# Kernel optimization log

Hardware: AMD Instinct MI355X
Metric: run time of the kernel (lower is better)

## Reference

```python
import jax, jax.numpy as jnp
import numpy as np

N_CONCEPTS = 32
KMEANS_ITERS = 10   # fixed Lloyd iterations (stand-in for fit-to-convergence)
CC_ITERS = 20       # label-propagation + pointer-jumping iterations (>= ~2*log2(N))


def setup_inputs() -> dict:
    key = jax.random.key(0)
    k1, k2, k3, k4 = jax.random.split(key, 4)
    B, N, F = 16, 512, 256
    x = jax.random.normal(k1, (B, N, F), dtype=jnp.float32)
    # sparse symmetric 0/1 adjacency, no self loops, avg degree ~20
    u = jax.random.uniform(k2, (B, N, N))
    a = (u < 0.02).astype(jnp.float32)
    adj = jnp.clip(a + jnp.swapaxes(a, 1, 2), 0.0, 1.0)
    adj = adj * (1.0 - jnp.eye(N, dtype=jnp.float32))
    mask = jnp.ones((B, N), dtype=bool)
    s = 1.0 / np.sqrt(F)
    W1 = jax.random.normal(k3, (F, F), jnp.float32) * s
    b1 = jnp.zeros((F,), jnp.float32)
    W2 = jax.random.normal(k4, (F, F), jnp.float32) * s
    b2 = jnp.zeros((F,), jnp.float32)
    return {"x": x, "adj": adj, "mask": mask, "W1": W1, "b1": b1, "W2": W2, "b2": b2}


def _gcn(x, adj, mask, W, b):
    # DenseGCNConv: D^-1/2 (A+I) D^-1/2 (X W) + b, masked
    N = x.shape[1]
    h = x @ W
    a = adj + jnp.eye(N, dtype=adj.dtype)
    d = jnp.clip(a.sum(-1), 1.0, None) ** -0.5
    a = d[:, :, None] * a * d[:, None, :]
    out = jnp.einsum('bij,bjf->bif', a, h) + b
    return jnp.where(mask[:, :, None], out, 0.0)


def _kmeans_fit_predict(pts, k):
    # Lloyd iterations, euclidean; deterministic init = first k points
    cent = pts[:k]
    p2 = (pts * pts).sum(-1)
    for _ in range(KMEANS_ITERS):
        d2 = p2[:, None] - 2.0 * pts @ cent.T + (cent * cent).sum(-1)[None]
        assign = jnp.argmin(d2, -1)
        sums = jax.ops.segment_sum(pts, assign, num_segments=k)
        cnt = jax.ops.segment_sum(jnp.ones_like(p2), assign, num_segments=k)
        cent = jnp.where(cnt[:, None] > 0, sums / jnp.maximum(cnt, 1.0)[:, None], cent)
    d2 = p2[:, None] - 2.0 * pts @ cent.T + (cent * cent).sum(-1)[None]
    return jnp.argmin(d2, -1)


def _components(adj_same, mask):
    # connected components of same-concept subgraph; returns 1-based cluster ids (0 = masked)
    B, N, _ = adj_same.shape
    idx = jnp.arange(N)
    labels = jnp.broadcast_to(idx[None, :], (B, N))
    A = adj_same > 0

    def step(lab, _):
        nb = jnp.where(A, lab[:, None, :], N)        # [B,N,N] neighbor labels
        lab = jnp.minimum(lab, nb.min(-1))           # hook to min neighbor
        lab = jnp.take_along_axis(lab, lab, axis=1)  # pointer jump
        lab = jnp.take_along_axis(lab, lab, axis=1)
        return lab, None

    labels, _ = jax.lax.scan(step, labels, None, length=CC_ITERS)
    is_root = mask & (labels == idx[None, :])
    ids = jnp.cumsum(is_root.astype(jnp.int32), axis=1)   # consecutive ids, 1-based at roots
    assign = jnp.take_along_axis(ids, labels, axis=1)
    return jnp.where(mask, assign, 0)


def _forward(x, adj, mask, W1, b1, W2, b2):
    B, N, F = x.shape
    h = jax.nn.relu(_gcn(x, adj, mask, W1, b1))
    h = jax.nn.relu(_gcn(h, adj, mask, W2, b2))
    # mask is all-true -> x[mask] is a flat reshape
    pts = jax.lax.stop_gradient(h.reshape(B * N, F))
    concepts = _kmeans_fit_predict(pts, N_CONCEPTS).reshape(B, N)
    adj_same = jnp.where(concepts[:, :, None] == concepts[:, None, :], adj, 0.0)
    assignments = _components(adj_same, mask)           # [B,N] in {0..N}
    seg_sum = jax.vmap(lambda v, s: jax.ops.segment_sum(v, s, num_segments=N + 1))
    x_new = seg_sum(h, assignments)[:, 1:, :]           # drop reserved cluster 0
    seg_max = jax.vmap(lambda v, s: jax.ops.segment_max(v, s, num_segments=N + 1))
    adj_r = jnp.maximum(seg_max(adj, assignments), 0.0)[:, 1:, :]                      # pool rows
    adj_new = jnp.maximum(seg_max(jnp.swapaxes(adj_r, 1, 2), assignments), 0.0)[:, 1:, :]
    adj_new = jnp.swapaxes(adj_new, 1, 2)                                              # pool cols
    num_clusters = assignments.max(-1)
    mask_new = jnp.arange(N)[None, :] < num_clusters[:, None]
    return x_new, adj_new, concepts, h, mask_new


def reference(x, adj, mask, W1, b1, W2, b2):
    return _forward(x, adj, mask, W1, b1, W2, b2)
```

## Files before the change

### kernel.cpp

```cpp
#include <hip/hip_runtime.h>
#include <cstdint>
#include <cstddef>

#define BB 16
#define NN 512
#define FF 256
#define NC 32
#define KITERS 10
#define CCITERS 20
#define MAXD 96
#define FMAXD 64

typedef __attribute__((ext_vector_type(4))) double double4_t;

__global__ __launch_bounds__(64) void build_adjbits(const float* __restrict__ adj,
                                                    unsigned long long* __restrict__ adjbits,
                                                    double* __restrict__ dinv,
                                                    unsigned short* __restrict__ nbr,
                                                    int* __restrict__ degv) {
  int i = blockIdx.x, b = blockIdx.y, lane = threadIdx.x;
  const float* row = adj + ((size_t)(b * NN + i)) * NN;
  unsigned long long lmask = (1ULL << lane) - 1ULL;
  int base = 0;
#pragma unroll
  for (int q = 0; q < 8; ++q) {
    bool pred = (row[q * 64 + lane] != 0.0f);
    unsigned long long m = __ballot(pred ? 1 : 0);
    if (lane == 0) adjbits[((size_t)(b * NN + i)) * 8 + q] = m;
    if (pred) {
      int pos = base + __popcll(m & lmask);
      if (pos < MAXD) nbr[((size_t)(b * NN + i)) * MAXD + pos] = (unsigned short)(q * 64 + lane);
    }
    base += __popcll(m);
  }
  if (lane == 0) {
    degv[b * NN + i] = base;
    double tot = (double)base + 1.0;
    dinv[b * NN + i] = 1.0 / sqrt(tot);
  }
}

__global__ __launch_bounds__(256) void gemm_scale(const float* __restrict__ X,
                                                  const float* __restrict__ W,
                                                  const double* __restrict__ dinv,
                                                  float* __restrict__ Y) {
  __shared__ float As[16][68];
  __shared__ float Bs[16][64];
  int bm = blockIdx.x, bn = blockIdx.y, b = blockIdx.z;
  int tid = threadIdx.x;
  int tx = tid & 15, ty = tid >> 4;
  const float* Xb = X + (size_t)b * NN * FF;
  float* Yb = Y + (size_t)b * NN * FF;
  double acc[4][4] = {};
  for (int kt = 0; kt < FF; kt += 16) {
    {
      int m = tid >> 2, kq = (tid & 3) * 4;
      const float4 v = *(const float4*)&Xb[(size_t)(bm * 64 + m) * FF + kt + kq];
      As[kq + 0][m] = v.x; As[kq + 1][m] = v.y; As[kq + 2][m] = v.z; As[kq + 3][m] = v.w;
    }
    {
      int k = tid >> 4, n4 = (tid & 15) * 4;
      *(float4*)&Bs[k][n4] = *(const float4*)&W[(size_t)(kt + k) * FF + bn * 64 + n4];
    }
    __syncthreads();
#pragma unroll
    for (int k = 0; k < 16; ++k) {
      float4 a = *(const float4*)&As[k][ty * 4];
      float4 bv = *(const float4*)&Bs[k][tx * 4];
      double ax = a.x, ay = a.y, az = a.z, aw = a.w;
      double bx = bv.x, by = bv.y, bz = bv.z, bw = bv.w;
      acc[0][0] += ax * bx; acc[0][1] += ax * by; acc[0][2] += ax * bz; acc[0][3] += ax * bw;
      acc[1][0] += ay * bx; acc[1][1] += ay * by; acc[1][2] += ay * bz; acc[1][3] += ay * bw;
      acc[2][0] += az * bx; acc[2][1] += az * by; acc[2][2] += az * bz; acc[2][3] += az * bw;
      acc[3][0] += aw * bx; acc[3][1] += aw * by; acc[3][2] += aw * bz; acc[3][3] += aw * bw;
    }
    __syncthreads();
  }
#pragma unroll
  for (int i = 0; i < 4; ++i) {
    int row = bm * 64 + ty * 4 + i;
    double di = dinv[b * NN + row];
    float4 v;
    v.x = (float)(di * acc[i][0]); v.y = (float)(di * acc[i][1]);
    v.z = (float)(di * acc[i][2]); v.w = (float)(di * acc[i][3]);
    *(float4*)&Yb[(size_t)row * FF + bn * 64 + tx * 4] = v;
  }
}

__global__ __launch_bounds__(256) void spmv_relu(const float* __restrict__ Y,
                                                 const unsigned short* __restrict__ nbr,
                                                 const int* __restrict__ degv,
                                                 const unsigned long long* __restrict__ adjbits,
                                                 const double* __restrict__ dinv,
                                                 const float* __restrict__ bias,
                                                 float* __restrict__ H) {
  int i = blockIdx.x, b = blockIdx.y, f = threadIdx.x;
  int row = b * NN + i;
  const float* Yb = Y + (size_t)b * NN * FF;
  double z = (double)Yb[(size_t)i * FF + f];
  int deg = degv[row];
  if (deg <= MAXD) {
    const unsigned short* lst = nbr + (size_t)row * MAXD;
    int n = 0;
    for (; n + 4 <= deg; n += 4) {
      int j0 = lst[n], j1 = lst[n + 1], j2 = lst[n + 2], j3 = lst[n + 3];
      float v0 = Yb[(size_t)j0 * FF + f];
      float v1 = Yb[(size_t)j1 * FF + f];
      float v2 = Yb[(size_t)j2 * FF + f];
      float v3 = Yb[(size_t)j3 * FF + f];
      z += (double)v0; z += (double)v1; z += (double)v2; z += (double)v3;
    }
    for (; n < deg; ++n) z += (double)Yb[(size_t)lst[n] * FF + f];
  } else {
    const unsigned long long* brow = adjbits + (size_t)row * 8;
    for (int q = 0; q < 8; ++q) {
      unsigned long long bits = brow[q];
      while (bits) {
        int j = (q << 6) + __builtin_ctzll(bits);
        bits &= bits - 1;
        z += (double)Yb[(size_t)j * FF + f];
      }
    }
  }
  double h = dinv[row] * z + (double)bias[f];
  H[((size_t)row) * FF + f] = (h > 0.0) ? (float)h : 0.0f;
}

__global__ __launch_bounds__(256) void p2cent_kernel(const float* __restrict__ pts,
                                                     double* __restrict__ p2,
                                                     double* __restrict__ cent,
                                                     double* __restrict__ c2) {
  __shared__ double red[256];
  int p = blockIdx.x, t = threadIdx.x;
  double v = (double)pts[(size_t)p * FF + t];
  if (p < NC) cent[p * FF + t] = v;
  red[t] = v * v;
  __syncthreads();
  for (int s = 128; s; s >>= 1) { if (t < s) red[t] += red[t + s]; __syncthreads(); }
  if (t == 0) {
    p2[p] = red[0];
    if (p < NC) c2[p] = red[0];
  }
}

__global__ __launch_bounds__(256) void kmeans_assign(const float* __restrict__ pts,
                                                     const double* __restrict__ cent,
                                                     const double* __restrict__ c2,
                                                     const double* __restrict__ p2,
                                                     int* __restrict__ assignI,
                                                     double* __restrict__ part,
                                                     int* __restrict__ cntp,
                                                     float* __restrict__ conceptsF) {
  __shared__ float ps[32][260];
  __shared__ double csT[256][35];
  __shared__ double d2s[32][33];
  __shared__ double want[3];
  __shared__ double probe_raw[2][2];
  __shared__ int as[32];
  __shared__ int hyp;
  int g = blockIdx.x, tid = threadIdx.x;

  for (int r = 0; r < 32; ++r) ps[r][tid] = pts[(size_t)(g * 32 + r) * FF + tid];
  for (int rep = 0; rep < 32; ++rep) csT[tid][rep] = cent[rep * FF + tid];
  __syncthreads();

  int lane = tid & 63, w = tid >> 6;
  int prow = (w >> 1) * 16, ccol = (w & 1) * 16;
  int r16 = lane & 15, kg = lane >> 4;
  double4_t acc = {0.0, 0.0, 0.0, 0.0};
  for (int kt = 0; kt < FF; kt += 4) {
    double a = (double)ps[prow + r16][kt + kg];
    double bv = csT[kt + kg][ccol + r16];
    acc = __builtin_amdgcn_mfma_f64_16x16x4f64(a, bv, acc, 0, 0, 0);
  }
  if (tid < 2) { probe_raw[tid][0] = acc[0]; probe_raw[tid][1] = acc[1]; }
  __syncthreads();

  if (tid < 192) {
    int pw = tid >> 6;
    int pr = (pw == 2) ? 1 : 0;
    int pc = (pw == 1) ? 1 : 0;
    double partial = 0.0;
#pragma unroll
    for (int kk = 0; kk < 4; ++kk)
      partial += (double)ps[pr][lane * 4 + kk] * csT[lane * 4 + kk][pc];
    for (int off = 32; off; off >>= 1) partial += __shfl_xor(partial, off, 64);
    if (lane == 0) want[pw] = partial;
  }
  __syncthreads();
  if (tid == 0) {
    double w00 = want[0], w01 = want[1], w10 = want[2];
    double m00 = probe_raw[0][0], mA = probe_raw[1][0], mB = probe_raw[0][1];
    auto near = [](double a, double b) { return fabs(a - b) <= 1e-9 * (1.0 + fabs(b)); };
    bool ok00 = near(m00, w00);
    bool h1 = ok00 && near(mA, w01) && near(mB, w10);
    bool h2 = ok00 && near(mB, w01) && near(mA, w10);
    hyp = h1 ? 0 : (h2 ? 1 : 2);
  }
  __syncthreads();
  int hh = hyp;
  if (hh == 0) {
#pragma unroll
    for (int ii = 0; ii < 4; ++ii) {
      int row = prow + kg * 4 + ii, col = ccol + r16;
      d2s[row][col] = (p2[g * 32 + row] - 2.0 * acc[ii]) + c2[col];
    }
  } else if (hh == 1) {
#pragma unroll
    for (int ii = 0; ii < 4; ++ii) {
      int row = prow + r16, col = ccol + kg * 4 + ii;
      d2s[row][col] = (p2[g * 32 + row] - 2.0 * acc[ii]) + c2[col];
    }
  }
  __syncthreads();
  if (hh == 2) {
    int p0 = tid >> 4, c0 = tid & 15;
    double a00 = 0., a01 = 0., a10 = 0., a11 = 0.;
    for (int k = 0; k < FF; ++k) {
      double pa = (double)ps[p0][k], pb = (double)ps[p0 + 16][k];
      double ca = csT[k][c0], cb = csT[k][c0 + 16];
      a00 += pa * ca; a01 += pa * cb; a10 += pb * ca; a11 += pb * cb;
    }
    double pp0 = p2[g * 32 + p0], pp1 = p2[g * 32 + p0 + 16];
    double cc0 = c2[c0], cc1 = c2[c0 + 16];
    d2s[p0][c0]           = (pp0 - 2.0 * a00) + cc0;
    d2s[p0][c0 + 16]      = (pp0 - 2.0 * a01) + cc1;
    d2s[p0 + 16][c0]      = (pp1 - 2.0 * a10) + cc0;
    d2s[p0 + 16][c0 + 16] = (pp1 - 2.0 * a11) + cc1;
  }
  __syncthreads();

  if (tid < 32) {
    double m = d2s[tid][0];
    int idx = 0;
    for (int c = 1; c < 32; ++c) {
      double v = d2s[tid][c];
      if (v < m) { m = v; idx = c; }
    }
    as[tid] = idx;
    assignI[g * 32 + tid] = idx;
    if (conceptsF) conceptsF[g * 32 + tid] = (float)idx;
  }
  double* accm = &csT[0][0];
  for (int r = 0; r < 32; ++r) accm[r * 258 + tid] = 0.0;
  __syncthreads();
  for (int r = 0; r < 32; ++r) { int s = as[r]; accm[s * 258 + tid] += (double)ps[r][tid]; }
  for (int r = 0; r < 32; ++r) part[((size_t)r * 256 + g) * FF + tid] = accm[r * 258 + tid];
  if (tid < 32) {
    int c = 0;
    for (int r = 0; r < 32; ++r) c += (as[r] == tid) ? 1 : 0;
    cntp[tid * 256 + g] = c;
  }
}

__global__ __launch_bounds__(256) void kmeans_update(const double* __restrict__ part,
                                                     const int* __restrict__ cntp,
                                                     double* __restrict__ cent,
                                                     double* __restrict__ c2) {
  __shared__ double red[256];
  int k = blockIdx.x, f = threadIdx.x;
  double s0 = 0., s1 = 0., s2 = 0., s3 = 0.;
  for (int g = 0; g < 256; g += 4) {
    s0 += part[((size_t)k * 256 + g + 0) * FF + f];
    s1 += part[((size_t)k * 256 + g + 1) * FF + f];
    s2 += part[((size_t)k * 256 + g + 2) * FF + f];
    s3 += part[((size_t)k * 256 + g + 3) * FF + f];
  }
  double acc = (s0 + s1) + (s2 + s3);
  int cnt = 0;
  for (int g = 0; g < 256; ++g) cnt += cntp[k * 256 + g];
  double v = (cnt > 0) ? (acc / (double)cnt) : cent[k * FF + f];
  cent[k * FF + f] = v;
  red[f] = v * v;
  __syncthreads();
  for (int s = 128; s; s >>= 1) { if (f < s) red[f] += red[f + s]; __syncthreads(); }
  if (f == 0) c2[k] = red[0];
}

__global__ __launch_bounds__(64) void build_bits(const unsigned long long* __restrict__ adjbits,
                                                 const int* __restrict__ concepts,
                                                 unsigned short* __restrict__ flistT,
                                                 int* __restrict__ fdegv) {
  int i = blockIdx.x, b = blockIdx.y, lane = threadIdx.x;
  int ci = concepts[b * NN + i];
  unsigned long long lmask = (1ULL << lane) - 1ULL;
  int base = 0;
#pragma unroll
  for (int q = 0; q < 8; ++q) {
    unsigned long long wbits = adjbits[((size_t)(b * NN + i)) * 8 + q];
    bool pred = ((wbits >> lane) & 1ULL) && (concepts[b * NN + q * 64 + lane] == ci);
    unsigned long long m = __ballot(pred ? 1 : 0);
    if (pred) {
      int pos = base + __popcll(m & lmask);
      if (pos < FMAXD) flistT[((size_t)b * FMAXD + pos) * NN + i] = (unsigned short)(q * 64 + lane);
    }
    base += __popcll(m);
  }
  if (lane == 0) fdegv[b * NN + i] = base;
}

__global__ __launch_bounds__(512) void components_kernel(const unsigned short* __restrict__ flistT,
                                                         const int* __restrict__ fdegv,
                                                         int* __restrict__ comp,
                                                         float* __restrict__ maskF) {
  __shared__ unsigned short LT[FMAXD][512];
  __shared__ int lab[512];
  __shared__ int ids[512];
  int b = blockIdx.x, t = threadIdx.x;
  for (int n = 0; n < FMAXD; ++n) LT[n][t] = flistT[((size_t)b * FMAXD + n) * NN + t];
  int fd = fdegv[b * NN + t];
  if (fd > FMAXD) fd = FMAXD;
  lab[t] = t;
  __syncthreads();
  for (int it = 0; it < CCITERS; ++it) {
    int old = lab[t];
    int m = old;
    for (int n = 0; n < fd; ++n) m = min(m, lab[LT[n][t]]);
    __syncthreads();
    lab[t] = m;
    __syncthreads();
    int a = lab[m];
    __syncthreads();
    lab[t] = a;
    __syncthreads();
    int a2 = lab[a];
    __syncthreads();
    lab[t] = a2;
    int changed = (a2 != old) ? 1 : 0;
    if (__syncthreads_or(changed) == 0) break;
  }
  if (t == 0) {
    int run = 0;
    for (int i = 0; i < 512; ++i) { run += (lab[i] == i) ? 1 : 0; ids[i] = run; }
  }
  __syncthreads();
  comp[b * NN + t] = ids[lab[t]];
  maskF[b * NN + t] = (t < ids[511]) ? 1.0f : 0.0f;
}

__global__ __launch_bounds__(256) void xnew_kernel(const float* __restrict__ H,
                                                   const int* __restrict__ comp,
                                                   float* __restrict__ xnew) {
  int i = blockIdx.x, b = blockIdx.y, f = threadIdx.x;
  int s = comp[b * NN + i] - 1;
  atomicAdd(&xnew[((size_t)(b * NN + s)) * FF + f], H[((size_t)(b * NN + i)) * FF + f]);
}

__global__ __launch_bounds__(64) void adjnew_kernel(const unsigned long long* __restrict__ adjbits,
                                                    const int* __restrict__ comp,
                                                    float* __restrict__ out) {
  int b = blockIdx.y, lane = threadIdx.x;
  int i = blockIdx.x * 8 + (lane >> 3);
  int q = lane & 7;
  unsigned long long bits = adjbits[((size_t)(b * NN + i)) * 8 + q];
  if (!bits) return;
  int si = comp[b * NN + i] - 1;
  float* ob = out + (size_t)b * NN * NN;
  while (bits) {
    int j = (q << 6) + __builtin_ctzll(bits);
    bits &= bits - 1;
    int sj = comp[b * NN + j] - 1;
    ob[(size_t)si * NN + sj] = 1.0f;
  }
}

extern "C" void kernel_launch(void* const* d_in, const int* in_sizes, int n_in,
                              void* d_out, int out_size, void* d_ws, size_t ws_size,
                              hipStream_t stream) {
  (void)in_sizes; (void)n_in; (void)out_size; (void)ws_size;
  const float* x   = (const float*)d_in[0];
  const float* adj = (const float*)d_in[1];
  const float* W1 = (const float*)d_in[3];
  const float* b1 = (const float*)d_in[4];
  const float* W2 = (const float*)d_in[5];
  const float* b2 = (const float*)d_in[6];

  float* out = (float*)d_out;
  float* xnew      = out;
  float* adjnew    = out + 2097152;
  float* conceptsF = out + 6291456;
  float* hout      = out + 6299648;
  float* maskF     = out + 8396800;

  char* ws = (char*)d_ws;
  double* dinv = (double*)(ws + 0);
  float*  y    = (float*)(ws + 65536);
  float*  h1   = (float*)(ws + 8454144);
  double* cent = (double*)(ws + 16842752);
  double* c2   = (double*)(ws + 16908288);
  double* p2   = (double*)(ws + 16908544);
  unsigned long long* adjbits = (unsigned long long*)(ws + 16974080);
  int* assignI = (int*)(ws + 17498368);
  int* cntp    = (int*)(ws + 17531136);
  int* comp    = (int*)(ws + 17563904);
  int* degv    = assignI;
  double* part = (double*)adjnew;
  unsigned short* nbr = (unsigned short*)xnew;
  unsigned short* flistT = (unsigned short*)h1;
  int* fdegv = (int*)(ws + 8454144 + 2097152);

  build_adjbits<<<dim3(NN, BB), 64, 0, stream>>>(adj, adjbits, dinv, nbr, degv);

  gemm_scale<<<dim3(8, 4, BB), 256, 0, stream>>>(x, W1, dinv, y);
  spmv_relu<<<dim3(NN, BB), 256, 0, stream>>>(y, nbr, degv, adjbits, dinv, b1, h1);
  gemm_scale<<<dim3(8, 4, BB), 256, 0, stream>>>(h1, W2, dinv, y);
  spmv_relu<<<dim3(NN, BB), 256, 0, stream>>>(y, nbr, degv, adjbits, dinv, b2, hout);

  hipMemsetAsync(xnew, 0, (size_t)2097152 * sizeof(float), stream);

  const float* pts = hout;
  p2cent_kernel<<<BB * NN, 256, 0, stream>>>(pts, p2, cent, c2);
  for (int it = 0; it < KITERS; ++it) {
    kmeans_assign<<<256, 256, 0, stream>>>(pts, cent, c2, p2, assignI, part, cntp, nullptr);
    kmeans_update<<<NC, 256, 0, stream>>>(part, cntp, cent, c2);
  }
  kmeans_assign<<<256, 256, 0, stream>>>(pts, cent, c2, p2, assignI, part, cntp, conceptsF);

  hipMemsetAsync(adjnew, 0, (size_t)4194304 * sizeof(float), stream);

  build_bits<<<dim3(NN, BB), 64, 0, stream>>>(adjbits, assignI, flistT, fdegv);
  components_kernel<<<BB, 512, 0, stream>>>(flistT, fdegv, comp, maskF);

  xnew_kernel<<<dim3(NN, BB), 256, 0, stream>>>(hout, comp, xnew);
  adjnew_kernel<<<dim3(64, BB), 64, 0, stream>>>(adjbits, comp, adjnew);
}
```

Before: 695.4 us.

## Split k-means centroid update across feature chunks and compute centroid norms in assign

```diff
diff --git a/kernel.cpp b/kernel.cpp
--- a/kernel.cpp
+++ b/kernel.cpp
@@ -128,8 +128,7 @@
 
 __global__ __launch_bounds__(256) void p2cent_kernel(const float* __restrict__ pts,
                                                      double* __restrict__ p2,
-                                                     double* __restrict__ cent,
-                                                     double* __restrict__ c2) {
+                                                     double* __restrict__ cent) {
   __shared__ double red[256];
   int p = blockIdx.x, t = threadIdx.x;
   double v = (double)pts[(size_t)p * FF + t];
@@ -137,15 +136,11 @@
   red[t] = v * v;
   __syncthreads();
   for (int s = 128; s; s >>= 1) { if (t < s) red[t] += red[t + s]; __syncthreads(); }
-  if (t == 0) {
-    p2[p] = red[0];
-    if (p < NC) c2[p] = red[0];
-  }
+  if (t == 0) p2[p] = red[0];
 }
 
 __global__ __launch_bounds__(256) void kmeans_assign(const float* __restrict__ pts,
                                                      const double* __restrict__ cent,
-                                                     const double* __restrict__ c2,
                                                      const double* __restrict__ p2,
                                                      int* __restrict__ assignI,
                                                      double* __restrict__ part,
@@ -154,6 +149,7 @@
   __shared__ float ps[32][260];
   __shared__ double csT[256][35];
   __shared__ double d2s[32][33];
+  __shared__ double c2s[32];
   __shared__ double want[3];
   __shared__ double probe_raw[2][2];
   __shared__ int as[32];
@@ -163,6 +159,12 @@
   for (int r = 0; r < 32; ++r) ps[r][tid] = pts[(size_t)(g * 32 + r) * FF + tid];
   for (int rep = 0; rep < 32; ++rep) csT[tid][rep] = cent[rep * FF + tid];
   __syncthreads();
+
+  if (tid < 32) {
+    double s = 0.;
+    for (int k = 0; k < FF; ++k) { double cv = csT[k][tid]; s += cv * cv; }
+    c2s[tid] = s;
+  }
 
   int lane = tid & 63, w = tid >> 6;
   int prow = (w >> 1) * 16, ccol = (w & 1) * 16;
@@ -203,13 +205,13 @@
 #pragma unroll
     for (int ii = 0; ii < 4; ++ii) {
       int row = prow + kg * 4 + ii, col = ccol + r16;
-      d2s[row][col] = (p2[g * 32 + row] - 2.0 * acc[ii]) + c2[col];
+      d2s[row][col] = (p2[g * 32 + row] - 2.0 * acc[ii]) + c2s[col];
     }
   } else if (hh == 1) {
 #pragma unroll
     for (int ii = 0; ii < 4; ++ii) {
       int row = prow + r16, col = ccol + kg * 4 + ii;
-      d2s[row][col] = (p2[g * 32 + row] - 2.0 * acc[ii]) + c2[col];
+      d2s[row][col] = (p2[g * 32 + row] - 2.0 * acc[ii]) + c2s[col];
     }
   }
   __syncthreads();
@@ -222,7 +224,7 @@
       a00 += pa * ca; a01 += pa * cb; a10 += pb * ca; a11 += pb * cb;
     }
     double pp0 = p2[g * 32 + p0], pp1 = p2[g * 32 + p0 + 16];
-    double cc0 = c2[c0], cc1 = c2[c0 + 16];
+    double cc0 = c2s[c0], cc1 = c2s[c0 + 16];
     d2s[p0][c0]           = (pp0 - 2.0 * a00) + cc0;
     d2s[p0][c0 + 16]      = (pp0 - 2.0 * a01) + cc1;
     d2s[p0 + 16][c0]      = (pp1 - 2.0 * a10) + cc0;
@@ -255,26 +257,29 @@
 
 __global__ __launch_bounds__(256) void kmeans_update(const double* __restrict__ part,
                                                      const int* __restrict__ cntp,
-                                                     double* __restrict__ cent,
-                                                     double* __restrict__ c2) {
-  __shared__ double red[256];
-  int k = blockIdx.x, f = threadIdx.x;
-  double s0 = 0., s1 = 0., s2 = 0., s3 = 0.;
-  for (int g = 0; g < 256; g += 4) {
-    s0 += part[((size_t)k * 256 + g + 0) * FF + f];
-    s1 += part[((size_t)k * 256 + g + 1) * FF + f];
-    s2 += part[((size_t)k * 256 + g + 2) * FF + f];
-    s3 += part[((size_t)k * 256 + g + 3) * FF + f];
-  }
-  double acc = (s0 + s1) + (s2 + s3);
-  int cnt = 0;
-  for (int g = 0; g < 256; ++g) cnt += cntp[k * 256 + g];
-  double v = (cnt > 0) ? (acc / (double)cnt) : cent[k * FF + f];
-  cent[k * FF + f] = v;
-  red[f] = v * v;
-  __syncthreads();
-  for (int s = 128; s; s >>= 1) { if (f < s) red[f] += red[f + s]; __syncthreads(); }
-  if (f == 0) c2[k] = red[0];
+                                                     double* __restrict__ cent) {
+  __shared__ double red[8][33];
+  __shared__ int cred[256];
+  int k = blockIdx.x, fc = blockIdx.y;
+  int tid = threadIdx.x;
+  int fl = tid & 31, gl = tid >> 5;
+  int f = fc * 32 + fl;
+  double s = 0.;
+  for (int gg = 0; gg < 32; ++gg) {
+    int g = gl + gg * 8;
+    s += part[((size_t)k * 256 + g) * FF + f];
+  }
+  red[gl][fl] = s;
+  cred[tid] = cntp[k * 256 + tid];
+  __syncthreads();
+  for (int q = 128; q; q >>= 1) { if (tid < q) cred[tid] += cred[tid + q]; __syncthreads(); }
+  if (gl == 0) {
+    double acc = 0.;
+    for (int q = 0; q < 8; ++q) acc += red[q][fl];
+    int cnt = cred[0];
+    double v = (cnt > 0) ? (acc / (double)cnt) : cent[k * FF + f];
+    cent[k * FF + f] = v;
+  }
 }
 
 __global__ __launch_bounds__(64) void build_bits(const unsigned long long* __restrict__ adjbits,
@@ -387,7 +392,6 @@
   float*  y    = (float*)(ws + 65536);
   float*  h1   = (float*)(ws + 8454144);
   double* cent = (double*)(ws + 16842752);
-  double* c2   = (double*)(ws + 16908288);
   double* p2   = (double*)(ws + 16908544);
   unsigned long long* adjbits = (unsigned long long*)(ws + 16974080);
   int* assignI = (int*)(ws + 17498368);
@@ -409,12 +413,12 @@
   hipMemsetAsync(xnew, 0, (size_t)2097152 * sizeof(float), stream);
 
   const float* pts = hout;
-  p2cent_kernel<<<BB * NN, 256, 0, stream>>>(pts, p2, cent, c2);
+  p2cent_kernel<<<BB * NN, 256, 0, stream>>>(pts, p2, cent);
   for (int it = 0; it < KITERS; ++it) {
-    kmeans_assign<<<256, 256, 0, stream>>>(pts, cent, c2, p2, assignI, part, cntp, nullptr);
-    kmeans_update<<<NC, 256, 0, stream>>>(part, cntp, cent, c2);
-  }
-  kmeans_assign<<<256, 256, 0, stream>>>(pts, cent, c2, p2, assignI, part, cntp, conceptsF);
+    kmeans_assign<<<256, 256, 0, stream>>>(pts, cent, p2, assignI, part, cntp, nullptr);
+    kmeans_update<<<dim3(NC, 8), 256, 0, stream>>>(part, cntp, cent);
+  }
+  kmeans_assign<<<256, 256, 0, stream>>>(pts, cent, p2, assignI, part, cntp, conceptsF);
 
   hipMemsetAsync(adjnew, 0, (size_t)4194304 * sizeof(float), stream);
 
```

Measured after the change: 629.2 us. -9.5%, faster.
